# Performance work log

Measured on AMD Instinct MI355X. Metric: run time of the kernel, lower is better.

Reference implementation:

```python
import jax, jax.numpy as jnp
import numpy as np

DIM = 512
NUM_HEADS = 8
HEAD_DIM = DIM // NUM_HEADS
SCALE = HEAD_DIM ** -0.5


def setup_inputs() -> dict:
    key = jax.random.key(0)
    kx, kqw, kqb, kpw, kpb = jax.random.split(key, 5)
    B, N = 2, 4096
    x = jax.random.normal(kx, (B, N, DIM), dtype=jnp.float32)
    # nn.Linear weights stored as [out, in]; init ~ U(-1/sqrt(in), 1/sqrt(in))
    bound = 1.0 / np.sqrt(DIM)
    qkv_w = jax.random.uniform(kqw, (3 * DIM, DIM), minval=-bound, maxval=bound, dtype=jnp.float32)
    qkv_b = jax.random.uniform(kqb, (3 * DIM,), minval=-bound, maxval=bound, dtype=jnp.float32)
    proj_w = jax.random.uniform(kpw, (DIM, DIM), minval=-bound, maxval=bound, dtype=jnp.float32)
    proj_b = jax.random.uniform(kpb, (DIM,), minval=-bound, maxval=bound, dtype=jnp.float32)
    return {"x": x, "qkv_w": qkv_w, "qkv_b": qkv_b, "proj_w": proj_w, "proj_b": proj_b}


def reference(x, qkv_w, qkv_b, proj_w, proj_b):
    B, N, C = x.shape
    # qkv: [B, N, 3C] -> [3, B, H, N, Dh]
    qkv = x @ qkv_w.T + qkv_b
    qkv = qkv.reshape(B, N, 3, NUM_HEADS, HEAD_DIM).transpose(2, 0, 3, 1, 4)
    q, k, v = qkv[0], qkv[1], qkv[2]
    # scores: [B, H, N, N] (materialized, matching the original math)
    attn = jnp.einsum("bhqd,bhkd->bhqk", q, k) * SCALE
    attn = jax.nn.softmax(attn, axis=-1)
    out = jnp.einsum("bhqk,bhkd->bhqd", attn, v)  # [B, H, N, Dh]
    out = out.transpose(0, 2, 1, 3).reshape(B, N, C)
    return out @ proj_w.T + proj_b
```

## Files before the change

kernel.cpp:

```cpp
#include <hip/hip_runtime.h>
#include <stdint.h>
#include <stddef.h>

typedef __attribute__((ext_vector_type(8))) short short8;
typedef __attribute__((ext_vector_type(4))) float f32x4;

#define MFMA16(a, b, c) __builtin_amdgcn_mfma_f32_16x16x32_bf16((a), (b), (c), 0, 0, 0)

__device__ __forceinline__ float b2f(short x) {
    unsigned u = ((unsigned)(unsigned short)x) << 16;
    float f; __builtin_memcpy(&f, &u, 4); return f;
}
__device__ __forceinline__ short f2b(float f) {
    unsigned u; __builtin_memcpy(&u, &f, 4);
    u = (u + 0x7FFFu + ((u >> 16) & 1u)) >> 16;
    return (short)u;
}
__device__ __forceinline__ unsigned pack2(float a, float b) {
    unsigned ua, ub; __builtin_memcpy(&ua, &a, 4); __builtin_memcpy(&ub, &b, 4);
    return __builtin_amdgcn_perm(ub + 0x8000u, ua + 0x8000u, 0x07060302u);
}
__device__ __forceinline__ short8 load8f(const float* p) {
    const float4 f0 = *(const float4*)p;
    const float4 f1 = *(const float4*)(p + 4);
    short8 r;
    r[0]=f2b(f0.x); r[1]=f2b(f0.y); r[2]=f2b(f0.z); r[3]=f2b(f0.w);
    r[4]=f2b(f1.x); r[5]=f2b(f1.y); r[6]=f2b(f1.z); r[7]=f2b(f1.w);
    return r;
}

__global__ __launch_bounds__(256) void cvt3(
    const float* __restrict__ s0, short* __restrict__ d0, int n0,
    const float* __restrict__ s1, short* __restrict__ d1, int n1,
    const float* __restrict__ s2, short* __restrict__ d2, int n2)
{
    int i = blockIdx.x * 256 + threadIdx.x;
    if (i < n0) { *(short8*)(d0 + (size_t)i * 8) = load8f(s0 + (size_t)i * 8); return; }
    i -= n0;
    if (i < n1) { *(short8*)(d1 + (size_t)i * 8) = load8f(s1 + (size_t)i * 8); return; }
    i -= n1;
    if (i < n2) { *(short8*)(d2 + (size_t)i * 8) = load8f(s2 + (size_t)i * 8); }
}

__global__ __launch_bounds__(256) void qkv_qk(
    const short* __restrict__ X, const short* __restrict__ W,
    const float* __restrict__ bias,
    short* __restrict__ Qb, short* __restrict__ Kb)
{
    const int tid  = threadIdx.x;
    const int wv   = tid >> 6;
    const int lane = tid & 63;
    const int l15  = lane & 15;
    const int quad = lane >> 4;
    const int m0   = blockIdx.x * 128 + (wv >> 1) * 64;
    const int sec  = blockIdx.y >> 2;
    const int bis  = blockIdx.y & 3;
    const int nbase = sec * 512 + bis * 128;
    const int j0   = (wv & 1) * 64;

    const f32x4 zero = {0.f, 0.f, 0.f, 0.f};
    f32x4 acc[4][4];
#pragma unroll
    for (int i = 0; i < 4; i++)
#pragma unroll
        for (int j = 0; j < 4; j++) acc[i][j] = zero;

    for (int k0 = 0; k0 < 512; k0 += 32) {
        short8 a[4], b[4];
#pragma unroll
        for (int i = 0; i < 4; i++)
            a[i] = *(const short8*)(X + (size_t)(m0 + i * 16 + l15) * 512 + k0 + quad * 8);
#pragma unroll
        for (int j = 0; j < 4; j++)
            b[j] = *(const short8*)(W + (size_t)(nbase + j0 + j * 16 + l15) * 512 + k0 + quad * 8);
#pragma unroll
        for (int i = 0; i < 4; i++)
#pragma unroll
            for (int j = 0; j < 4; j++)
                acc[i][j] = MFMA16(a[i], b[j], acc[i][j]);
    }

#pragma unroll
    for (int j = 0; j < 4; j++) {
        const int jc = bis * 128 + j0 + j * 16 + l15;
        const float bs = bias[sec * 512 + jc];
        const int hl = jc >> 6, d = jc & 63;
#pragma unroll
        for (int i = 0; i < 4; i++) {
#pragma unroll
            for (int r = 0; r < 4; r++) {
                const int m = m0 + i * 16 + quad * 4 + r;
                const int bb = m >> 12, seq = m & 4095;
                const int bh = bb * 8 + hl;
                const float v = acc[i][j][r] + bs;
                if (sec == 0)
                    Qb[((size_t)bh * 4096 + seq) * 64 + d] = f2b(v * 0.125f);
                else
                    Kb[((size_t)bh * 4096 + seq) * 64 + d] = f2b(v);
            }
        }
    }
}

__global__ __launch_bounds__(256) void qkv_v(
    const short* __restrict__ X, const short* __restrict__ W,
    const float* __restrict__ bias, short* __restrict__ Vb)
{
    __shared__ short sT[128][132];

    const int tid  = threadIdx.x;
    const int wv   = tid >> 6;
    const int lane = tid & 63;
    const int l15  = lane & 15;
    const int quad = lane >> 4;
    const int m0   = blockIdx.x * 128 + (wv >> 1) * 64;
    const int bis  = blockIdx.y;
    const int nbase = 1024 + bis * 128;
    const int j0   = (wv & 1) * 64;

    const f32x4 zero = {0.f, 0.f, 0.f, 0.f};
    f32x4 acc[4][4];
#pragma unroll
    for (int i = 0; i < 4; i++)
#pragma unroll
        for (int j = 0; j < 4; j++) acc[i][j] = zero;

    for (int k0 = 0; k0 < 512; k0 += 32) {
        short8 a[4], b[4];
#pragma unroll
        for (int i = 0; i < 4; i++)
            a[i] = *(const short8*)(X + (size_t)(m0 + i * 16 + l15) * 512 + k0 + quad * 8);
#pragma unroll
        for (int j = 0; j < 4; j++)
            b[j] = *(const short8*)(W + (size_t)(nbase + j0 + j * 16 + l15) * 512 + k0 + quad * 8);
#pragma unroll
        for (int i = 0; i < 4; i++)
#pragma unroll
            for (int j = 0; j < 4; j++)
                acc[i][j] = MFMA16(a[i], b[j], acc[i][j]);
    }

#pragma unroll
    for (int j = 0; j < 4; j++) {
        const int jcl = j0 + j * 16 + l15;
        const float bs = bias[nbase + jcl];
#pragma unroll
        for (int i = 0; i < 4; i++) {
            uint2 w;
            w.x = pack2(acc[i][j][0] + bs, acc[i][j][1] + bs);
            w.y = pack2(acc[i][j][2] + bs, acc[i][j][3] + bs);
            *(uint2*)&sT[jcl][(wv >> 1) * 64 + i * 16 + quad * 4] = w;
        }
    }
    __syncthreads();

    const int jcl = tid >> 1, half = tid & 1;
    const int hl = (bis * 128 + jcl) >> 6;
    const int d  = jcl & 63;
    const int bb = (blockIdx.x * 128) >> 12;
    const int seq0 = ((blockIdx.x * 128) & 4095) + half * 64;
    short* dst = Vb + ((size_t)(bb * 8 + hl) * 64 + d) * 4096 + seq0;
#pragma unroll
    for (int u = 0; u < 8; u++)
        *(short8*)(dst + u * 8) = *(const short8*)&sT[jcl][half * 64 + u * 8];
}

__global__ __launch_bounds__(256) void flash_attn(
    const short* __restrict__ Q, const short* __restrict__ K,
    const short* __restrict__ V, short* __restrict__ PO0,
    short* __restrict__ PO1, float* __restrict__ lbuf, int ktiles)
{
    __shared__ short sK[64][72];
    __shared__ short sV[64][72];
    __shared__ short sP[4][2][16][72];

    const int tid  = threadIdx.x;
    const int wv   = tid >> 6;
    const int lane = tid & 63;
    const int l15  = lane & 15;
    const int quad = lane >> 4;
    const int bh = blockIdx.y;
    const int b = bh >> 3, h = bh & 7;
    const int qw = blockIdx.x * 128 + wv * 32;
    const int ks = blockIdx.z;
    const int key0 = ks * ktiles * 64;

    const short* Qb = Q + (size_t)bh * 4096 * 64;
    const short* Kb = K + (size_t)bh * 4096 * 64;
    const short* Vb = V + (size_t)bh * 64 * 4096;

    const short8 aq00 = *(const short8*)(Qb + (size_t)(qw + l15) * 64 + quad * 8);
    const short8 aq01 = *(const short8*)(Qb + (size_t)(qw + l15) * 64 + 32 + quad * 8);
    const short8 aq10 = *(const short8*)(Qb + (size_t)(qw + 16 + l15) * 64 + quad * 8);
    const short8 aq11 = *(const short8*)(Qb + (size_t)(qw + 16 + l15) * 64 + 32 + quad * 8);

    const f32x4 zero = {0.f, 0.f, 0.f, 0.f};
    f32x4 o0[4], o1[4];
    float l0 = 0.f, l1 = 0.f;
#pragma unroll
    for (int r = 0; r < 4; r++) { o0[r] = zero; o1[r] = zero; }

    int srow[2], scb[2];
#pragma unroll
    for (int i = 0; i < 2; i++) {
        const int c = tid + i * 256;
        srow[i] = c >> 3; scb[i] = (c & 7) * 8;
    }

    short8 pk[2], pv[2];
#pragma unroll
    for (int i = 0; i < 2; i++) {
        pk[i] = *(const short8*)(Kb + (size_t)(key0 + srow[i]) * 64 + scb[i]);
        pv[i] = *(const short8*)(Vb + (size_t)srow[i] * 4096 + key0 + scb[i]);
    }

    for (int kt = 0; kt < ktiles; ++kt) {
        const int k0 = key0 + kt * 64;
        __syncthreads();
#pragma unroll
        for (int i = 0; i < 2; i++) {
            *(short8*)&sK[srow[i]][scb[i]] = pk[i];
            *(short8*)&sV[srow[i]][scb[i]] = pv[i];
        }
        __syncthreads();

        if (kt + 1 < ktiles) {
            const int k0n = k0 + 64;
#pragma unroll
            for (int i = 0; i < 2; i++) {
                pk[i] = *(const short8*)(Kb + (size_t)(k0n + srow[i]) * 64 + scb[i]);
                pv[i] = *(const short8*)(Vb + (size_t)srow[i] * 4096 + k0n + scb[i]);
            }
        }

        f32x4 ST0[4], ST1[4];
#pragma unroll
        for (int c = 0; c < 4; c++) {
            const short8 bk0 = *(const short8*)&sK[c * 16 + l15][quad * 8];
            const short8 bk1 = *(const short8*)&sK[c * 16 + l15][32 + quad * 8];
            ST0[c] = MFMA16(bk1, aq01, MFMA16(bk0, aq00, zero));
            ST1[c] = MFMA16(bk1, aq11, MFMA16(bk0, aq10, zero));
        }

#pragma unroll
        for (int c = 0; c < 4; c++) {
            const float p0 = __expf(ST0[c][0]), p1 = __expf(ST0[c][1]);
            const float p2 = __expf(ST0[c][2]), p3 = __expf(ST0[c][3]);
            l0 += (p0 + p1) + (p2 + p3);
            uint2 w; w.x = pack2(p0, p1); w.y = pack2(p2, p3);
            *(uint2*)&sP[wv][0][l15][c * 16 + quad * 4] = w;
            const float r0 = __expf(ST1[c][0]), r1 = __expf(ST1[c][1]);
            const float r2 = __expf(ST1[c][2]), r3 = __expf(ST1[c][3]);
            l1 += (r0 + r1) + (r2 + r3);
            uint2 v; v.x = pack2(r0, r1); v.y = pack2(r2, r3);
            *(uint2*)&sP[wv][1][l15][c * 16 + quad * 4] = v;
        }
        __threadfence_block();

        const short8 bp00 = *(const short8*)&sP[wv][0][l15][quad * 8];
        const short8 bp01 = *(const short8*)&sP[wv][0][l15][32 + quad * 8];
        const short8 bp10 = *(const short8*)&sP[wv][1][l15][quad * 8];
        const short8 bp11 = *(const short8*)&sP[wv][1][l15][32 + quad * 8];

#pragma unroll
        for (int td = 0; td < 4; td++) {
            const short8 bv0 = *(const short8*)&sV[td * 16 + l15][quad * 8];
            const short8 bv1 = *(const short8*)&sV[td * 16 + l15][32 + quad * 8];
            o0[td] = MFMA16(bv0, bp00, o0[td]);
            o0[td] = MFMA16(bv1, bp01, o0[td]);
            o1[td] = MFMA16(bv0, bp10, o1[td]);
            o1[td] = MFMA16(bv1, bp11, o1[td]);
        }
    }

    l0 += __shfl_xor(l0, 16); l0 += __shfl_xor(l0, 32);
    l1 += __shfl_xor(l1, 16); l1 += __shfl_xor(l1, 32);
    const float inv0 = 1.f / fmaxf(l0, 1e-30f);
    const float inv1 = 1.f / fmaxf(l1, 1e-30f);

    short* PO = (ks == 0) ? PO0 : PO1;
#pragma unroll
    for (int td = 0; td < 4; td++) {
        uint2 w0, w1;
        w0.x = pack2(o0[td][0] * inv0, o0[td][1] * inv0);
        w0.y = pack2(o0[td][2] * inv0, o0[td][3] * inv0);
        w1.x = pack2(o1[td][0] * inv1, o1[td][1] * inv1);
        w1.y = pack2(o1[td][2] * inv1, o1[td][3] * inv1);
        const int col = h * 64 + td * 16 + quad * 4;
        *(uint2*)(PO + ((size_t)b * 4096 + qw + l15) * 512 + col) = w0;
        *(uint2*)(PO + ((size_t)b * 4096 + qw + 16 + l15) * 512 + col) = w1;
    }
    if (lbuf && quad == 0) {
        lbuf[((size_t)ks * 16 + bh) * 4096 + qw + l15] = l0;
        lbuf[((size_t)ks * 16 + bh) * 4096 + qw + 16 + l15] = l1;
    }
}

__global__ __launch_bounds__(256) void combine(
    const short* __restrict__ PO0, short* __restrict__ PO1,
    const float* __restrict__ L)
{
    const int i = blockIdx.x * 256 + threadIdx.x;
    const size_t flat = (size_t)i * 8;
    const int col = (int)(flat & 511);
    const int q   = (int)((flat >> 9) & 4095);
    const int b   = (int)(flat >> 21);
    const int bh  = b * 8 + (col >> 6);
    const float l0 = L[(size_t)bh * 4096 + q];
    const float l1 = L[(size_t)65536 + (size_t)bh * 4096 + q];
    const float inv = 1.f / (l0 + l1);
    const float w0 = l0 * inv, w1 = l1 * inv;
    const short8 a = *(const short8*)(PO0 + flat);
    const short8 c = *(const short8*)(PO1 + flat);
    short8 r;
#pragma unroll
    for (int k = 0; k < 8; k++) r[k] = f2b(w0 * b2f(a[k]) + w1 * b2f(c[k]));
    *(short8*)(PO1 + flat) = r;
}

__global__ __launch_bounds__(256) void proj_piece(
    const short* __restrict__ A, const short* __restrict__ W,
    const float* __restrict__ bias, float* __restrict__ dst, int m_base)
{
    const int tid  = threadIdx.x;
    const int wv   = tid >> 6;
    const int lane = tid & 63;
    const int l15  = lane & 15;
    const int quad = lane >> 4;
    const int m0 = blockIdx.x * 128 + (wv >> 1) * 64;
    const int n0 = blockIdx.y * 128 + (wv & 1) * 64;

    const f32x4 zero = {0.f, 0.f, 0.f, 0.f};
    f32x4 acc[4][4];
#pragma unroll
    for (int i = 0; i < 4; i++)
#pragma unroll
        for (int j = 0; j < 4; j++) acc[i][j] = zero;

    for (int k0 = 0; k0 < 512; k0 += 32) {
        short8 a[4], b[4];
#pragma unroll
        for (int i = 0; i < 4; i++)
            a[i] = *(const short8*)(A + (size_t)(m_base + m0 + i * 16 + l15) * 512 + k0 + quad * 8);
#pragma unroll
        for (int j = 0; j < 4; j++)
            b[j] = *(const short8*)(W + (size_t)(n0 + j * 16 + l15) * 512 + k0 + quad * 8);
#pragma unroll
        for (int i = 0; i < 4; i++)
#pragma unroll
            for (int j = 0; j < 4; j++)
                acc[i][j] = MFMA16(a[i], b[j], acc[i][j]);
    }

#pragma unroll
    for (int j = 0; j < 4; j++) {
        const int n = n0 + j * 16 + l15;
        const float bs = bias[n];
#pragma unroll
        for (int i = 0; i < 4; i++) {
#pragma unroll
            for (int r = 0; r < 4; r++) {
                const int m = m0 + i * 16 + quad * 4 + r;
                dst[(size_t)m * 512 + n] = acc[i][j][r] + bs;
            }
        }
    }
}

extern "C" void kernel_launch(void* const* d_in, const int* in_sizes, int n_in,
                              void* d_out, int out_size, void* d_ws, size_t ws_size,
                              hipStream_t stream)
{
    const float* x      = (const float*)d_in[0];
    const float* qkv_w  = (const float*)d_in[1];
    const float* qkv_b  = (const float*)d_in[2];
    const float* proj_w = (const float*)d_in[3];
    const float* proj_b = (const float*)d_in[4];

    const size_t MB = 1024 * 1024;
    short* xb   = (short*)d_out;
    short* wb   = (short*)d_out + 4 * MB;
    short* attn = (short*)d_out + 4 * MB;
    float* out  = (float*)d_out;

    short* Qf = (short*)d_ws;
    short* Kf = Qf + (size_t)16 * 4096 * 64;
    short* Vf = Kf + (size_t)16 * 4096 * 64;
    float* lbuf = (float*)((char*)d_ws + 24 * MB);
    short* pwb  = (short*)((char*)d_ws + 24 * MB + 512 * 1024);

    cvt3<<<2560, 256, 0, stream>>>(x, xb, 524288, qkv_w, wb, 98304, proj_w, pwb, 32768);
    qkv_qk<<<dim3(64, 8), 256, 0, stream>>>(xb, wb, qkv_b, Qf, Kf);
    qkv_v <<<dim3(64, 4), 256, 0, stream>>>(xb, wb, qkv_b, Vf);
    flash_attn<<<dim3(32, 16, 2), 256, 0, stream>>>(Qf, Kf, Vf, (short*)d_out, attn, lbuf, 32);
    combine<<<2048, 256, 0, stream>>>((const short*)d_out, attn, lbuf);
    proj_piece<<<dim3(32, 4), 256, 0, stream>>>(attn, pwb, proj_b, out, 0);
    proj_piece<<<dim3(32, 4), 256, 0, stream>>>(attn, pwb, proj_b, (float*)d_ws, 4096);
    hipMemcpyAsync((char*)d_out + 8 * MB, d_ws, 8 * MB,
                   hipMemcpyDeviceToDevice, stream);
}
```

Baseline: 281.7 us.

## Merge QKV kernels, widen flash-attention tiles, fold combine into projection

The Q/K and V projection kernels are merged into one launch that branches on the output section. Flash attention now has each wave handle 64 query rows instead of 32. It computes exp2 with log2(e) folded into the Q scale and gets row sums from an MFMA against a ones vector instead of scalar adds. The separate combine kernel is removed: the projection GEMM blends the two key-split partial outputs while loading its A operand, and the output is copied in one 16 MB memcpy. This cuts launches and a full pass over the intermediate, but the blend is now recomputed for every output-column tile, and the wider attention tiles raise register pressure and halve the number of blocks.

```diff
diff --git a/kernel.cpp b/kernel.cpp
--- a/kernel.cpp
+++ b/kernel.cpp
@@ -1,4 +1,5 @@
 #include <hip/hip_runtime.h>
+#include <hip/hip_bf16.h>
 #include <stdint.h>
 #include <stddef.h>
 
@@ -6,6 +7,8 @@
 typedef __attribute__((ext_vector_type(4))) float f32x4;
 
 #define MFMA16(a, b, c) __builtin_amdgcn_mfma_f32_16x16x32_bf16((a), (b), (c), 0, 0, 0)
+
+#define QSCALE 0.1803368801111204f
 
 __device__ __forceinline__ float b2f(short x) {
     unsigned u = ((unsigned)(unsigned short)x) << 16;
@@ -16,9 +19,9 @@
     u = (u + 0x7FFFu + ((u >> 16) & 1u)) >> 16;
     return (short)u;
 }
-__device__ __forceinline__ unsigned pack2(float a, float b) {
-    unsigned ua, ub; __builtin_memcpy(&ua, &a, 4); __builtin_memcpy(&ub, &b, 4);
-    return __builtin_amdgcn_perm(ub + 0x8000u, ua + 0x8000u, 0x07060302u);
+__device__ __forceinline__ unsigned pkrn(float a, float b) {
+    __hip_bfloat162 h = __float22bfloat162_rn(float2{a, b});
+    unsigned u; __builtin_memcpy(&u, &h, 4); return u;
 }
 __device__ __forceinline__ short8 load8f(const float* p) {
     const float4 f0 = *(const float4*)p;
@@ -42,11 +45,13 @@
     if (i < n2) { *(short8*)(d2 + (size_t)i * 8) = load8f(s2 + (size_t)i * 8); }
 }
 
-__global__ __launch_bounds__(256) void qkv_qk(
+__global__ __launch_bounds__(256) void qkv_gemm(
     const short* __restrict__ X, const short* __restrict__ W,
     const float* __restrict__ bias,
-    short* __restrict__ Qb, short* __restrict__ Kb)
-{
+    short* __restrict__ Qb, short* __restrict__ Kb, short* __restrict__ Vb)
+{
+    __shared__ short sT[128][132];
+
     const int tid  = threadIdx.x;
     const int wv   = tid >> 6;
     const int lane = tid & 63;
@@ -80,99 +85,60 @@
                 acc[i][j] = MFMA16(a[i], b[j], acc[i][j]);
     }
 
-#pragma unroll
-    for (int j = 0; j < 4; j++) {
-        const int jc = bis * 128 + j0 + j * 16 + l15;
-        const float bs = bias[sec * 512 + jc];
-        const int hl = jc >> 6, d = jc & 63;
-#pragma unroll
-        for (int i = 0; i < 4; i++) {
-#pragma unroll
-            for (int r = 0; r < 4; r++) {
-                const int m = m0 + i * 16 + quad * 4 + r;
-                const int bb = m >> 12, seq = m & 4095;
-                const int bh = bb * 8 + hl;
-                const float v = acc[i][j][r] + bs;
-                if (sec == 0)
-                    Qb[((size_t)bh * 4096 + seq) * 64 + d] = f2b(v * 0.125f);
-                else
-                    Kb[((size_t)bh * 4096 + seq) * 64 + d] = f2b(v);
-            }
-        }
-    }
-}
-
-__global__ __launch_bounds__(256) void qkv_v(
-    const short* __restrict__ X, const short* __restrict__ W,
-    const float* __restrict__ bias, short* __restrict__ Vb)
-{
-    __shared__ short sT[128][132];
-
-    const int tid  = threadIdx.x;
-    const int wv   = tid >> 6;
-    const int lane = tid & 63;
-    const int l15  = lane & 15;
-    const int quad = lane >> 4;
-    const int m0   = blockIdx.x * 128 + (wv >> 1) * 64;
-    const int bis  = blockIdx.y;
-    const int nbase = 1024 + bis * 128;
-    const int j0   = (wv & 1) * 64;
-
-    const f32x4 zero = {0.f, 0.f, 0.f, 0.f};
-    f32x4 acc[4][4];
-#pragma unroll
-    for (int i = 0; i < 4; i++)
-#pragma unroll
-        for (int j = 0; j < 4; j++) acc[i][j] = zero;
-
-    for (int k0 = 0; k0 < 512; k0 += 32) {
-        short8 a[4], b[4];
-#pragma unroll
-        for (int i = 0; i < 4; i++)
-            a[i] = *(const short8*)(X + (size_t)(m0 + i * 16 + l15) * 512 + k0 + quad * 8);
-#pragma unroll
-        for (int j = 0; j < 4; j++)
-            b[j] = *(const short8*)(W + (size_t)(nbase + j0 + j * 16 + l15) * 512 + k0 + quad * 8);
-#pragma unroll
-        for (int i = 0; i < 4; i++)
-#pragma unroll
-            for (int j = 0; j < 4; j++)
-                acc[i][j] = MFMA16(a[i], b[j], acc[i][j]);
-    }
-
-#pragma unroll
-    for (int j = 0; j < 4; j++) {
-        const int jcl = j0 + j * 16 + l15;
-        const float bs = bias[nbase + jcl];
-#pragma unroll
-        for (int i = 0; i < 4; i++) {
-            uint2 w;
-            w.x = pack2(acc[i][j][0] + bs, acc[i][j][1] + bs);
-            w.y = pack2(acc[i][j][2] + bs, acc[i][j][3] + bs);
-            *(uint2*)&sT[jcl][(wv >> 1) * 64 + i * 16 + quad * 4] = w;
-        }
-    }
-    __syncthreads();
-
-    const int jcl = tid >> 1, half = tid & 1;
-    const int hl = (bis * 128 + jcl) >> 6;
-    const int d  = jcl & 63;
-    const int bb = (blockIdx.x * 128) >> 12;
-    const int seq0 = ((blockIdx.x * 128) & 4095) + half * 64;
-    short* dst = Vb + ((size_t)(bb * 8 + hl) * 64 + d) * 4096 + seq0;
-#pragma unroll
-    for (int u = 0; u < 8; u++)
-        *(short8*)(dst + u * 8) = *(const short8*)&sT[jcl][half * 64 + u * 8];
-}
-
-__global__ __launch_bounds__(256) void flash_attn(
+    if (sec < 2) {
+        const float scale = (sec == 0) ? QSCALE : 1.0f;
+        short* dst = (sec == 0) ? Qb : Kb;
+#pragma unroll
+        for (int j = 0; j < 4; j++) {
+            const int jc = bis * 128 + j0 + j * 16 + l15;
+            const float bs = bias[sec * 512 + jc];
+            const int hl = jc >> 6, d = jc & 63;
+#pragma unroll
+            for (int i = 0; i < 4; i++) {
+#pragma unroll
+                for (int r = 0; r < 4; r++) {
+                    const int m = m0 + i * 16 + quad * 4 + r;
+                    const int bb = m >> 12, seq = m & 4095;
+                    dst[((size_t)(bb * 8 + hl) * 4096 + seq) * 64 + d] =
+                        f2b((acc[i][j][r] + bs) * scale);
+                }
+            }
+        }
+    } else {
+#pragma unroll
+        for (int j = 0; j < 4; j++) {
+            const int jcl = j0 + j * 16 + l15;
+            const float bs = bias[nbase + jcl];
+#pragma unroll
+            for (int i = 0; i < 4; i++) {
+                uint2 w;
+                w.x = pkrn(acc[i][j][0] + bs, acc[i][j][1] + bs);
+                w.y = pkrn(acc[i][j][2] + bs, acc[i][j][3] + bs);
+                *(uint2*)&sT[jcl][(wv >> 1) * 64 + i * 16 + quad * 4] = w;
+            }
+        }
+        __syncthreads();
+
+        const int jcl = tid >> 1, half = tid & 1;
+        const int hl = (bis * 128 + jcl) >> 6;
+        const int d  = jcl & 63;
+        const int bb = (blockIdx.x * 128) >> 12;
+        const int seq0 = ((blockIdx.x * 128) & 4095) + half * 64;
+        short* dst = Vb + ((size_t)(bb * 8 + hl) * 64 + d) * 4096 + seq0;
+#pragma unroll
+        for (int u = 0; u < 8; u++)
+            *(short8*)(dst + u * 8) = *(const short8*)&sT[jcl][half * 64 + u * 8];
+    }
+}
+
+__global__ __launch_bounds__(256, 2) void flash_attn(
     const short* __restrict__ Q, const short* __restrict__ K,
     const short* __restrict__ V, short* __restrict__ PO0,
     short* __restrict__ PO1, float* __restrict__ lbuf, int ktiles)
 {
     __shared__ short sK[64][72];
     __shared__ short sV[64][72];
-    __shared__ short sP[4][2][16][72];
+    __shared__ short sP[4][16][72];
 
     const int tid  = threadIdx.x;
     const int wv   = tid >> 6;
@@ -181,7 +147,7 @@
     const int quad = lane >> 4;
     const int bh = blockIdx.y;
     const int b = bh >> 3, h = bh & 7;
-    const int qw = blockIdx.x * 128 + wv * 32;
+    const int qw = blockIdx.x * 256 + wv * 64;
     const int ks = blockIdx.z;
     const int key0 = ks * ktiles * 64;
 
@@ -189,16 +155,25 @@
     const short* Kb = K + (size_t)bh * 4096 * 64;
     const short* Vb = V + (size_t)bh * 64 * 4096;
 
-    const short8 aq00 = *(const short8*)(Qb + (size_t)(qw + l15) * 64 + quad * 8);
-    const short8 aq01 = *(const short8*)(Qb + (size_t)(qw + l15) * 64 + 32 + quad * 8);
-    const short8 aq10 = *(const short8*)(Qb + (size_t)(qw + 16 + l15) * 64 + quad * 8);
-    const short8 aq11 = *(const short8*)(Qb + (size_t)(qw + 16 + l15) * 64 + 32 + quad * 8);
+    short8 aq[4][2];
+#pragma unroll
+    for (int g = 0; g < 4; g++) {
+        const short* qp = Qb + (size_t)(qw + g * 16 + l15) * 64;
+        aq[g][0] = *(const short8*)(qp + quad * 8);
+        aq[g][1] = *(const short8*)(qp + 32 + quad * 8);
+    }
 
     const f32x4 zero = {0.f, 0.f, 0.f, 0.f};
-    f32x4 o0[4], o1[4];
-    float l0 = 0.f, l1 = 0.f;
-#pragma unroll
-    for (int r = 0; r < 4; r++) { o0[r] = zero; o1[r] = zero; }
+    f32x4 o[4][4];
+    f32x4 lac[4];
+#pragma unroll
+    for (int g = 0; g < 4; g++) {
+        lac[g] = zero;
+#pragma unroll
+        for (int td = 0; td < 4; td++) o[g][td] = zero;
+    }
+    const short one_bf = (short)0x3F80;
+    const short8 ones = {one_bf, one_bf, one_bf, one_bf, one_bf, one_bf, one_bf, one_bf};
 
     int srow[2], scb[2];
 #pragma unroll
@@ -206,7 +181,6 @@
         const int c = tid + i * 256;
         srow[i] = c >> 3; scb[i] = (c & 7) * 8;
     }
-
     short8 pk[2], pv[2];
 #pragma unroll
     for (int i = 0; i < 2; i++) {
@@ -233,93 +207,71 @@
             }
         }
 
-        f32x4 ST0[4], ST1[4];
+        short8 bk[4][2], bv[4][2];
 #pragma unroll
         for (int c = 0; c < 4; c++) {
-            const short8 bk0 = *(const short8*)&sK[c * 16 + l15][quad * 8];
-            const short8 bk1 = *(const short8*)&sK[c * 16 + l15][32 + quad * 8];
-            ST0[c] = MFMA16(bk1, aq01, MFMA16(bk0, aq00, zero));
-            ST1[c] = MFMA16(bk1, aq11, MFMA16(bk0, aq10, zero));
-        }
-
-#pragma unroll
-        for (int c = 0; c < 4; c++) {
-            const float p0 = __expf(ST0[c][0]), p1 = __expf(ST0[c][1]);
-            const float p2 = __expf(ST0[c][2]), p3 = __expf(ST0[c][3]);
-            l0 += (p0 + p1) + (p2 + p3);
-            uint2 w; w.x = pack2(p0, p1); w.y = pack2(p2, p3);
-            *(uint2*)&sP[wv][0][l15][c * 16 + quad * 4] = w;
-            const float r0 = __expf(ST1[c][0]), r1 = __expf(ST1[c][1]);
-            const float r2 = __expf(ST1[c][2]), r3 = __expf(ST1[c][3]);
-            l1 += (r0 + r1) + (r2 + r3);
-            uint2 v; v.x = pack2(r0, r1); v.y = pack2(r2, r3);
-            *(uint2*)&sP[wv][1][l15][c * 16 + quad * 4] = v;
-        }
-        __threadfence_block();
-
-        const short8 bp00 = *(const short8*)&sP[wv][0][l15][quad * 8];
-        const short8 bp01 = *(const short8*)&sP[wv][0][l15][32 + quad * 8];
-        const short8 bp10 = *(const short8*)&sP[wv][1][l15][quad * 8];
-        const short8 bp11 = *(const short8*)&sP[wv][1][l15][32 + quad * 8];
-
+            bk[c][0] = *(const short8*)&sK[c * 16 + l15][quad * 8];
+            bk[c][1] = *(const short8*)&sK[c * 16 + l15][32 + quad * 8];
+        }
 #pragma unroll
         for (int td = 0; td < 4; td++) {
-            const short8 bv0 = *(const short8*)&sV[td * 16 + l15][quad * 8];
-            const short8 bv1 = *(const short8*)&sV[td * 16 + l15][32 + quad * 8];
-            o0[td] = MFMA16(bv0, bp00, o0[td]);
-            o0[td] = MFMA16(bv1, bp01, o0[td]);
-            o1[td] = MFMA16(bv0, bp10, o1[td]);
-            o1[td] = MFMA16(bv1, bp11, o1[td]);
-        }
-    }
-
-    l0 += __shfl_xor(l0, 16); l0 += __shfl_xor(l0, 32);
-    l1 += __shfl_xor(l1, 16); l1 += __shfl_xor(l1, 32);
-    const float inv0 = 1.f / fmaxf(l0, 1e-30f);
-    const float inv1 = 1.f / fmaxf(l1, 1e-30f);
+            bv[td][0] = *(const short8*)&sV[td * 16 + l15][quad * 8];
+            bv[td][1] = *(const short8*)&sV[td * 16 + l15][32 + quad * 8];
+        }
+
+#pragma unroll
+        for (int g = 0; g < 4; g++) {
+            f32x4 ST[4];
+#pragma unroll
+            for (int c = 0; c < 4; c++)
+                ST[c] = MFMA16(bk[c][1], aq[g][1], MFMA16(bk[c][0], aq[g][0], zero));
+
+#pragma unroll
+            for (int c = 0; c < 4; c++) {
+                uint2 w;
+                w.x = pkrn(exp2f(ST[c][0]), exp2f(ST[c][1]));
+                w.y = pkrn(exp2f(ST[c][2]), exp2f(ST[c][3]));
+                *(uint2*)&sP[wv][l15][c * 16 + quad * 4] = w;
+            }
+            __threadfence_block();
+
+            const short8 bp0 = *(const short8*)&sP[wv][l15][quad * 8];
+            const short8 bp1 = *(const short8*)&sP[wv][l15][32 + quad * 8];
+
+            lac[g] = MFMA16(ones, bp0, lac[g]);
+            lac[g] = MFMA16(ones, bp1, lac[g]);
+
+#pragma unroll
+            for (int td = 0; td < 4; td++) {
+                o[g][td] = MFMA16(bv[td][0], bp0, o[g][td]);
+                o[g][td] = MFMA16(bv[td][1], bp1, o[g][td]);
+            }
+            __threadfence_block();
+        }
+    }
 
     short* PO = (ks == 0) ? PO0 : PO1;
 #pragma unroll
-    for (int td = 0; td < 4; td++) {
-        uint2 w0, w1;
-        w0.x = pack2(o0[td][0] * inv0, o0[td][1] * inv0);
-        w0.y = pack2(o0[td][2] * inv0, o0[td][3] * inv0);
-        w1.x = pack2(o1[td][0] * inv1, o1[td][1] * inv1);
-        w1.y = pack2(o1[td][2] * inv1, o1[td][3] * inv1);
-        const int col = h * 64 + td * 16 + quad * 4;
-        *(uint2*)(PO + ((size_t)b * 4096 + qw + l15) * 512 + col) = w0;
-        *(uint2*)(PO + ((size_t)b * 4096 + qw + 16 + l15) * 512 + col) = w1;
-    }
-    if (lbuf && quad == 0) {
-        lbuf[((size_t)ks * 16 + bh) * 4096 + qw + l15] = l0;
-        lbuf[((size_t)ks * 16 + bh) * 4096 + qw + 16 + l15] = l1;
-    }
-}
-
-__global__ __launch_bounds__(256) void combine(
-    const short* __restrict__ PO0, short* __restrict__ PO1,
-    const float* __restrict__ L)
-{
-    const int i = blockIdx.x * 256 + threadIdx.x;
-    const size_t flat = (size_t)i * 8;
-    const int col = (int)(flat & 511);
-    const int q   = (int)((flat >> 9) & 4095);
-    const int b   = (int)(flat >> 21);
-    const int bh  = b * 8 + (col >> 6);
-    const float l0 = L[(size_t)bh * 4096 + q];
-    const float l1 = L[(size_t)65536 + (size_t)bh * 4096 + q];
-    const float inv = 1.f / (l0 + l1);
-    const float w0 = l0 * inv, w1 = l1 * inv;
-    const short8 a = *(const short8*)(PO0 + flat);
-    const short8 c = *(const short8*)(PO1 + flat);
-    short8 r;
-#pragma unroll
-    for (int k = 0; k < 8; k++) r[k] = f2b(w0 * b2f(a[k]) + w1 * b2f(c[k]));
-    *(short8*)(PO1 + flat) = r;
+    for (int g = 0; g < 4; g++) {
+        const float l = lac[g][0];
+        const float inv = 1.f / fmaxf(l, 1e-30f);
+        const int seq = qw + g * 16 + l15;
+#pragma unroll
+        for (int td = 0; td < 4; td++) {
+            uint2 w;
+            w.x = pkrn(o[g][td][0] * inv, o[g][td][1] * inv);
+            w.y = pkrn(o[g][td][2] * inv, o[g][td][3] * inv);
+            const int col = h * 64 + td * 16 + quad * 4;
+            *(uint2*)(PO + ((size_t)b * 4096 + seq) * 512 + col) = w;
+        }
+        if (quad == 0)
+            lbuf[((size_t)ks * 16 + bh) * 4096 + seq] = l;
+    }
 }
 
 __global__ __launch_bounds__(256) void proj_piece(
-    const short* __restrict__ A, const short* __restrict__ W,
+    const short* __restrict__ PO0, const short* __restrict__ PO1,
+    const float* __restrict__ L, const short* __restrict__ W,
     const float* __restrict__ bias, float* __restrict__ dst, int m_base)
 {
     const int tid  = threadIdx.x;
@@ -338,10 +290,30 @@
         for (int j = 0; j < 4; j++) acc[i][j] = zero;
 
     for (int k0 = 0; k0 < 512; k0 += 32) {
+        const int head = (k0 + quad * 8) >> 6;
         short8 a[4], b[4];
 #pragma unroll
-        for (int i = 0; i < 4; i++)
-            a[i] = *(const short8*)(A + (size_t)(m_base + m0 + i * 16 + l15) * 512 + k0 + quad * 8);
+        for (int i = 0; i < 4; i++) {
+            const int row = m_base + m0 + i * 16 + l15;
+            const size_t off = (size_t)row * 512 + k0 + quad * 8;
+            const short8 a0 = *(const short8*)(PO0 + off);
+            const short8 a1 = *(const short8*)(PO1 + off);
+            const int bh = (row >> 12) * 8 + head;
+            const int q  = row & 4095;
+            const float l0 = L[(size_t)bh * 4096 + q];
+            const float l1 = L[(size_t)65536 + (size_t)bh * 4096 + q];
+            const float inv = 1.f / (l0 + l1);
+            const float w0 = l0 * inv, w1 = l1 * inv;
+            short8 av;
+#pragma unroll
+            for (int u = 0; u < 8; u += 2) {
+                const unsigned p = pkrn(w0 * b2f(a0[u]) + w1 * b2f(a1[u]),
+                                        w0 * b2f(a0[u + 1]) + w1 * b2f(a1[u + 1]));
+                av[u]     = (short)(p & 0xFFFF);
+                av[u + 1] = (short)(p >> 16);
+            }
+            a[i] = av;
+        }
 #pragma unroll
         for (int j = 0; j < 4; j++)
             b[j] = *(const short8*)(W + (size_t)(n0 + j * 16 + l15) * 512 + k0 + quad * 8);
@@ -378,10 +350,10 @@
     const float* proj_b = (const float*)d_in[4];
 
     const size_t MB = 1024 * 1024;
-    short* xb   = (short*)d_out;
-    short* wb   = (short*)d_out + 4 * MB;
-    short* attn = (short*)d_out + 4 * MB;
-    float* out  = (float*)d_out;
+    short* xb  = (short*)d_out;
+    short* wb  = (short*)d_out + 4 * MB;
+    short* PO0 = (short*)d_out;
+    short* PO1 = (short*)d_out + 4 * MB;
 
     short* Qf = (short*)d_ws;
     short* Kf = Qf + (size_t)16 * 4096 * 64;
@@ -390,12 +362,11 @@
     short* pwb  = (short*)((char*)d_ws + 24 * MB + 512 * 1024);
 
     cvt3<<<2560, 256, 0, stream>>>(x, xb, 524288, qkv_w, wb, 98304, proj_w, pwb, 32768);
-    qkv_qk<<<dim3(64, 8), 256, 0, stream>>>(xb, wb, qkv_b, Qf, Kf);
-    qkv_v <<<dim3(64, 4), 256, 0, stream>>>(xb, wb, qkv_b, Vf);
-    flash_attn<<<dim3(32, 16, 2), 256, 0, stream>>>(Qf, Kf, Vf, (short*)d_out, attn, lbuf, 32);
-    combine<<<2048, 256, 0, stream>>>((const short*)d_out, attn, lbuf);
-    proj_piece<<<dim3(32, 4), 256, 0, stream>>>(attn, pwb, proj_b, out, 0);
-    proj_piece<<<dim3(32, 4), 256, 0, stream>>>(attn, pwb, proj_b, (float*)d_ws, 4096);
-    hipMemcpyAsync((char*)d_out + 8 * MB, d_ws, 8 * MB,
-                   hipMemcpyDeviceToDevice, stream);
-}
+    qkv_gemm<<<dim3(64, 12), 256, 0, stream>>>(xb, wb, qkv_b, Qf, Kf, Vf);
+    flash_attn<<<dim3(16, 16, 2), 256, 0, stream>>>(Qf, Kf, Vf, PO0, PO1, lbuf, 32);
+    proj_piece<<<dim3(32, 4), 256, 0, stream>>>(PO0, PO1, lbuf, pwb, proj_b,
+                                                (float*)d_ws, 0);
+    proj_piece<<<dim3(32, 4), 256, 0, stream>>>(PO0, PO1, lbuf, pwb, proj_b,
+                                                (float*)((char*)d_ws + 8 * MB), 4096);
+    hipMemcpyAsync(d_out, d_ws, 16 * MB, hipMemcpyDeviceToDevice, stream);
+}
```

Result: slower. 314.8 us (+11.7%).
